# Kernel optimization log

Hardware: AMD Instinct MI355X
Metric: run time of the kernel (lower is better)

Reference implementation:

```python
import math
import jax, jax.numpy as jnp
import numpy as np

H = 8
D = 32  # c_hidden per head


def setup_inputs() -> dict:
    key = jax.random.key(0)
    ks = jax.random.split(key, 10)
    B, Q, K, C = 2, 2048, 2048, 256
    s = 1.0 / math.sqrt(C)
    return {
        "q_x": jax.random.normal(ks[0], (B, Q, C), jnp.float32),
        "kv_x": jax.random.normal(ks[1], (B, K, C), jnp.float32),
        "bias_mask": jax.random.normal(ks[2], (B, 1, 1, K), jnp.float32),
        "bias_pair": jax.random.normal(ks[3], (1, H, Q, K), jnp.float32),
        "Wq": jax.random.normal(ks[4], (H * D, C), jnp.float32) * s,
        "Wk": jax.random.normal(ks[5], (H * D, C), jnp.float32) * s,
        "Wv": jax.random.normal(ks[6], (H * D, C), jnp.float32) * s,
        "Wo": jax.random.normal(ks[7], (C, H * D), jnp.float32) * s,
        "bo": jnp.zeros((C,), jnp.float32),
        "Wg": jax.random.normal(ks[8], (H * D, C), jnp.float32) * s,
        "bg": jnp.zeros((H * D,), jnp.float32),
    }


def reference(q_x, kv_x, bias_mask, bias_pair, Wq, Wk, Wv, Wo, bo, Wg, bg):
    B, Q, C = q_x.shape
    K = kv_x.shape[-2]
    # projections (torch Linear: x @ W.T), split heads -> [B,H,L,D]
    q = (q_x @ Wq.T).reshape(B, Q, H, D).swapaxes(-2, -3) / math.sqrt(D)
    k = (kv_x @ Wk.T).reshape(B, K, H, D).swapaxes(-2, -3)
    v = (kv_x @ Wv.T).reshape(B, K, H, D).swapaxes(-2, -3)
    scores = jnp.einsum("bhqd,bhkd->bhqk", q, k) + bias_mask + bias_pair
    w = jax.nn.softmax(scores, axis=-1)
    o = jnp.einsum("bhqk,bhkd->bhqd", w, v).swapaxes(-2, -3)  # [B,Q,H,D]
    g = jax.nn.sigmoid(q_x @ Wg.T + bg).reshape(B, Q, H, D)
    o = o * g
    return o.reshape(B, Q, H * D) @ Wo.T + bo
```

## Files before the change

kernel.cpp:

```cpp
#include <hip/hip_runtime.h>
#include <hip/hip_bf16.h>
#include <stdint.h>
#include <math.h>

typedef __attribute__((ext_vector_type(8))) short bf16x8;
typedef __attribute__((ext_vector_type(4))) float f32x4;

#define HQ 2048
#define HK 2048
#define NH 8
#define ND 32
#define NC 256

union U8 { uint32_t u[4]; bf16x8 v; };

__device__ __forceinline__ uint16_t f2bf(float f) {
  uint32_t u = __float_as_uint(f);
  u += 0x7FFFu + ((u >> 16) & 1u);
  return (uint16_t)(u >> 16);
}
__device__ __forceinline__ uint32_t pack2bf(float a, float b) {
  return (uint32_t)f2bf(a) | ((uint32_t)f2bf(b) << 16);
}
__device__ __forceinline__ int swz64(int row, int piece) {
  int s = (((row >> 3) & 1) << 1) | ((row >> 1) & 1);
  return row * 64 + ((piece ^ s) << 4);
}
__device__ __forceinline__ f32x4 mfma32(bf16x8 a, bf16x8 b, f32x4 c) {
  return __builtin_amdgcn_mfma_f32_16x16x32_bf16(a, b, c, 0, 0, 0);
}
__device__ __forceinline__ void dma16(const void* g, void* l) {
  __builtin_amdgcn_global_load_lds(
      (const __attribute__((address_space(1))) uint32_t*)g,
      (__attribute__((address_space(3))) uint32_t*)l, 16, 0, 0);
}

__global__ __launch_bounds__(256) void proj_kernel(
    const float* __restrict__ qx, const float* __restrict__ kvx,
    const float* __restrict__ Wq, const float* __restrict__ Wk,
    const float* __restrict__ Wv, const float* __restrict__ Wg,
    const float* __restrict__ bg,
    uint16_t* __restrict__ q_p, uint16_t* __restrict__ k_p,
    uint16_t* __restrict__ v_p, float* __restrict__ g_ws)
{
  const int bx = blockIdx.x;
  const int Mb = bx & 63, Nb = (bx >> 6) & 3, p = bx >> 8;
  const int Mbase = Mb * 64, Nbase = Nb * 64;
  const float* X = (p == 0 || p == 3) ? qx : kvx;
  const float* W = (p == 0) ? Wq : (p == 1) ? Wk : (p == 2) ? Wv : Wg;

  __shared__ __align__(16) uint16_t smem[4096];
  uint16_t* sX = smem;
  uint16_t* sW = smem + 2048;

  const int tid = threadIdx.x;
  const int l = tid & 63, w = tid >> 6;
  const int qq = l & 15, g = l >> 4;
  const int row = tid >> 2, gp = tid & 3;

  f32x4 acc[4] = {};

  for (int ks = 0; ks < 8; ++ks) {
    const float* xs = X + (size_t)(Mbase + row) * 256 + ks * 32 + gp * 8;
    f32x4 x0 = *(const f32x4*)xs;
    f32x4 x1 = *(const f32x4*)(xs + 4);
    const float* ws_ = W + (size_t)(Nbase + row) * 256 + ks * 32 + gp * 8;
    f32x4 w0 = *(const f32x4*)ws_;
    f32x4 w1 = *(const f32x4*)(ws_ + 4);
    U8 ux, uw;
    ux.u[0] = pack2bf(x0[0], x0[1]); ux.u[1] = pack2bf(x0[2], x0[3]);
    ux.u[2] = pack2bf(x1[0], x1[1]); ux.u[3] = pack2bf(x1[2], x1[3]);
    uw.u[0] = pack2bf(w0[0], w0[1]); uw.u[1] = pack2bf(w0[2], w0[3]);
    uw.u[2] = pack2bf(w1[0], w1[1]); uw.u[3] = pack2bf(w1[2], w1[3]);
    __syncthreads();
    *(bf16x8*)((char*)sX + swz64(row, gp)) = ux.v;
    *(bf16x8*)((char*)sW + swz64(row, gp)) = uw.v;
    __syncthreads();
    bf16x8 a = *(bf16x8*)((char*)sX + swz64(w * 16 + qq, g));
#pragma unroll
    for (int nf = 0; nf < 4; ++nf) {
      bf16x8 bb = *(bf16x8*)((char*)sW + swz64(nf * 16 + qq, g));
      acc[nf] = mfma32(a, bb, acc[nf]);
    }
  }

  if (p == 2) {
    __syncthreads();
#pragma unroll
    for (int nf = 0; nf < 4; ++nf) {
      int n_loc = nf * 16 + qq;
#pragma unroll
      for (int r = 0; r < 4; ++r) {
        int m_loc = w * 16 + 4 * g + r;
        int byte = n_loc * 128 + ((((m_loc >> 3) ^ (n_loc & 7)) << 4)) + (m_loc & 7) * 2;
        *(uint16_t*)((char*)smem + byte) = f2bf(acc[nf][r]);
      }
    }
    __syncthreads();
    const int n_loc = tid >> 2, mp = tid & 3;
    const int ng = Nbase + n_loc;
    const int hh = ng >> 5, dd = ng & 31;
    const int bb_ = Mbase >> 11;
#pragma unroll
    for (int jj = 0; jj < 2; ++jj) {
      int piece = mp * 2 + jj;
      bf16x8 vv = *(bf16x8*)((char*)smem + n_loc * 128 + ((piece ^ (n_loc & 7)) << 4));
      int seq = (Mbase & 2047) + piece * 8;
      *(bf16x8*)(v_p + ((size_t)(bb_ * NH + hh) * ND + dd) * (size_t)HK + seq) = vv;
    }
    return;
  }

#pragma unroll
  for (int nf = 0; nf < 4; ++nf) {
    int n = Nbase + nf * 16 + qq;
#pragma unroll
    for (int r = 0; r < 4; ++r) {
      int m = Mbase + w * 16 + 4 * g + r;
      float val = acc[nf][r];
      if (p == 0) {
        val *= 0.17677669529663687f;
        int bb_ = m >> 11, seq = m & 2047, hh = n >> 5, dd = n & 31;
        q_p[((size_t)(bb_ * NH + hh) * HQ + seq) * ND + dd] = f2bf(val);
      } else if (p == 1) {
        int bb_ = m >> 11, seq = m & 2047, hh = n >> 5, dd = n & 31;
        k_p[((size_t)(bb_ * NH + hh) * HK + seq) * ND + dd] = f2bf(val);
      } else {
        g_ws[(size_t)m * NC + n] = 1.f / (1.f + __expf(-(val + bg[n])));
      }
    }
  }
}

__global__ __launch_bounds__(256, 2) void attn_kernel(
    const uint16_t* __restrict__ q_p, const uint16_t* __restrict__ k_p,
    const uint16_t* __restrict__ v_p, const float* __restrict__ bias_mask,
    const float* __restrict__ bias_pair,
    float* __restrict__ O_ws, float* __restrict__ l_ws)
{
  const int bx = blockIdx.x;
  const int kh = bx & 1, h = (bx >> 1) & 7, qt = bx >> 4;

  __shared__ __align__(16) char LDS[73728];
  char* sK = LDS;
  char* sV = LDS + 16384;
  char* sP = LDS + 32768;
  char* sBM = LDS + 65536;

  const int tid = threadIdx.x;
  const int l = tid & 63, wq = tid >> 6;
  const int qq = l & 15, g = l >> 4;
  const int q_glob = qt * 64 + wq * 16 + qq;

  bf16x8 qf0 = *(const bf16x8*)(q_p + ((size_t)h * HQ + q_glob) * ND + g * 8);
  bf16x8 qf1 = *(const bf16x8*)(q_p + ((size_t)(NH + h) * HQ + q_glob) * ND + g * 8);

  int kOffLane;
  {
    int B = wq * 1024 + l * 16;
    int Lr = B >> 7, q8 = l & 7;
    int hp = q8 ^ (Lr & 7);
    int half = hp >> 2, pc = hp & 3;
    int s = Lr * 2 + half, F = s >> 4, qs = s & 15;
    int krow = 8 * (qs >> 2) + (qs & 3) + (F & 1) * 4 + (F >> 1) * 32;
    kOffLane = krow * 64 + pc * 16;
  }
  const char* kSrc0 = (const char*)(k_p + (size_t)h * HK * ND) + kh * 65536 + kOffLane;
  const char* kSrc1 = (const char*)(k_p + (size_t)(NH + h) * HK * ND) + kh * 65536 + kOffLane;
  int vOffLane;
  {
    int B = wq * 1024 + l * 16;
    int d = B >> 7, q8 = l & 7;
    int pc = q8 ^ (d & 7);
    vOffLane = d * (HK * 2) + pc * 16;
  }
  const char* vSrc0 = (const char*)(v_p + (size_t)h * ND * (size_t)HK) + kh * 2048 + vOffLane;
  const char* vSrc1 = (const char*)(v_p + (size_t)(NH + h) * ND * (size_t)HK) + kh * 2048 + vOffLane;
  const char* pSrc0; const char* pSrc1; const char* pSrc2; const char* pSrc3;
  {
    const char* bpBlk = (const char*)bias_pair + ((size_t)h * HQ + qt * 64) * (size_t)HK * 4 + kh * 4096;
    int q16 = l & 15;
#define BP_SRC(jj) ({ int row = (wq * 4 + (jj)) * 4 + (l >> 4); \
                      int pc = (q16 & 8) | ((q16 & 7) ^ (row & 7)); \
                      bpBlk + (size_t)row * HK * 4 + pc * 16; })
    pSrc0 = BP_SRC(0); pSrc1 = BP_SRC(1); pSrc2 = BP_SRC(2); pSrc3 = BP_SRC(3);
#undef BP_SRC
  }

  int afOff[4], vaOff[4], bpOff[4];
#pragma unroll
  for (int F = 0; F < 4; ++F) {
    int Ls = 8 * F + (qq >> 1);
    afOff[F] = Ls * 128 + (((qq & 1) * 4 + g) ^ (qq >> 1)) * 16;
  }
#pragma unroll
  for (int hd = 0; hd < 2; ++hd)
#pragma unroll
    for (int c = 0; c < 2; ++c) {
      int d = hd * 16 + qq;
      vaOff[hd * 2 + c] = d * 128 + ((4 * c + g) ^ (d & 7)) * 16;
    }
#pragma unroll
  for (int F = 0; F < 4; ++F) {
    int piece = 8 * (F >> 1) + 2 * g + (F & 1);
    int row = wq * 16 + qq;
    bpOff[F] = row * 256 + ((piece & 8) | ((piece & 7) ^ (row & 7))) * 16;
  }

#define STAGE(tt, dbi) do { \
    dma16(kSrc0 + (size_t)(tt) * 4096, sK + (dbi) * 8192 + wq * 1024); \
    dma16(kSrc1 + (size_t)(tt) * 4096, sK + (dbi) * 8192 + 4096 + wq * 1024); \
    dma16(vSrc0 + (size_t)(tt) * 128,  sV + (dbi) * 8192 + wq * 1024); \
    dma16(vSrc1 + (size_t)(tt) * 128,  sV + (dbi) * 8192 + 4096 + wq * 1024); \
    dma16(pSrc0 + (size_t)(tt) * 256,  sP + (dbi) * 16384 + wq * 4096); \
    dma16(pSrc1 + (size_t)(tt) * 256,  sP + (dbi) * 16384 + wq * 4096 + 1024); \
    dma16(pSrc2 + (size_t)(tt) * 256,  sP + (dbi) * 16384 + wq * 4096 + 2048); \
    dma16(pSrc3 + (size_t)(tt) * 256,  sP + (dbi) * 16384 + wq * 4096 + 3072); \
  } while (0)

  f32x4 o00 = {}, o01 = {}, o10 = {}, o11 = {};
  float l0 = 0.f, l1 = 0.f;

  dma16((const char*)bias_mask + kh * 4096 + wq * 1024 + l * 16,
        sBM + wq * 1024);
  dma16((const char*)bias_mask + 8192 + kh * 4096 + wq * 1024 + l * 16,
        sBM + 4096 + wq * 1024);
  STAGE(0, 0);

#pragma unroll 1
  for (int t = 0; t < 16; ++t) {
    const int bi = t & 1;
    if (t < 15) {
      STAGE(t + 1, bi ^ 1);
      asm volatile("s_waitcnt vmcnt(8)" ::: "memory");
    } else {
      asm volatile("s_waitcnt vmcnt(0)" ::: "memory");
    }
    __builtin_amdgcn_s_barrier();
    __builtin_amdgcn_sched_barrier(0);

    const char* bP = sP + bi * 16384;
    f32x4 bp0 = *(const f32x4*)(bP + bpOff[0]);
    f32x4 bp1 = *(const f32x4*)(bP + bpOff[1]);
    f32x4 bp2 = *(const f32x4*)(bP + bpOff[2]);
    f32x4 bp3 = *(const f32x4*)(bP + bpOff[3]);
    const int bmOff = t * 256 + 32 * g;

    {
      const char* bK = sK + bi * 8192;
      const char* bV = sV + bi * 8192;
      bf16x8 af0 = *(const bf16x8*)(bK + afOff[0]);
      bf16x8 af1 = *(const bf16x8*)(bK + afOff[1]);
      bf16x8 af2 = *(const bf16x8*)(bK + afOff[2]);
      bf16x8 af3 = *(const bf16x8*)(bK + afOff[3]);
      f32x4 z = {};
      f32x4 s0 = mfma32(af0, qf0, z);
      f32x4 s1 = mfma32(af1, qf0, z);
      f32x4 s2 = mfma32(af2, qf0, z);
      f32x4 s3 = mfma32(af3, qf0, z);
      f32x4 bm0 = *(const f32x4*)(sBM + bmOff);
      f32x4 bm1 = *(const f32x4*)(sBM + bmOff + 16);
      f32x4 bm2 = *(const f32x4*)(sBM + bmOff + 128);
      f32x4 bm3 = *(const f32x4*)(sBM + bmOff + 144);
#pragma unroll
      for (int r = 0; r < 4; ++r) {
        s0[r] += bp0[r] + bm0[r];
        s1[r] += bp1[r] + bm1[r];
        s2[r] += bp2[r] + bm2[r];
        s3[r] += bp3[r] + bm3[r];
      }
      uint32_t pbk[4][2];
      {
        float p0 = __expf(s0[0]), p1 = __expf(s0[1]);
        float p2 = __expf(s0[2]), p3 = __expf(s0[3]);
        l0 += (p0 + p1) + (p2 + p3);
        pbk[0][0] = pack2bf(p0, p1); pbk[0][1] = pack2bf(p2, p3);
        p0 = __expf(s1[0]); p1 = __expf(s1[1]);
        p2 = __expf(s1[2]); p3 = __expf(s1[3]);
        l0 += (p0 + p1) + (p2 + p3);
        pbk[1][0] = pack2bf(p0, p1); pbk[1][1] = pack2bf(p2, p3);
        p0 = __expf(s2[0]); p1 = __expf(s2[1]);
        p2 = __expf(s2[2]); p3 = __expf(s2[3]);
        l0 += (p0 + p1) + (p2 + p3);
        pbk[2][0] = pack2bf(p0, p1); pbk[2][1] = pack2bf(p2, p3);
        p0 = __expf(s3[0]); p1 = __expf(s3[1]);
        p2 = __expf(s3[2]); p3 = __expf(s3[3]);
        l0 += (p0 + p1) + (p2 + p3);
        pbk[3][0] = pack2bf(p0, p1); pbk[3][1] = pack2bf(p2, p3);
      }
      U8 bu0, bu1;
      bu0.u[0] = pbk[0][0]; bu0.u[1] = pbk[0][1];
      bu0.u[2] = pbk[1][0]; bu0.u[3] = pbk[1][1];
      bu1.u[0] = pbk[2][0]; bu1.u[1] = pbk[2][1];
      bu1.u[2] = pbk[3][0]; bu1.u[3] = pbk[3][1];
      bf16x8 va00 = *(const bf16x8*)(bV + vaOff[0]);
      bf16x8 va01 = *(const bf16x8*)(bV + vaOff[1]);
      bf16x8 va10 = *(const bf16x8*)(bV + vaOff[2]);
      bf16x8 va11 = *(const bf16x8*)(bV + vaOff[3]);
      o00 = mfma32(va00, bu0.v, o00);
      o01 = mfma32(va10, bu0.v, o01);
      o00 = mfma32(va01, bu1.v, o00);
      o01 = mfma32(va11, bu1.v, o01);
    }
    {
      const char* bK = sK + bi * 8192 + 4096;
      const char* bV = sV + bi * 8192 + 4096;
      bf16x8 af0 = *(const bf16x8*)(bK + afOff[0]);
      bf16x8 af1 = *(const bf16x8*)(bK + afOff[1]);
      bf16x8 af2 = *(const bf16x8*)(bK + afOff[2]);
      bf16x8 af3 = *(const bf16x8*)(bK + afOff[3]);
      f32x4 z = {};
      f32x4 s0 = mfma32(af0, qf1, z);
      f32x4 s1 = mfma32(af1, qf1, z);
      f32x4 s2 = mfma32(af2, qf1, z);
      f32x4 s3 = mfma32(af3, qf1, z);
      f32x4 bm0 = *(const f32x4*)(sBM + 4096 + bmOff);
      f32x4 bm1 = *(const f32x4*)(sBM + 4096 + bmOff + 16);
      f32x4 bm2 = *(const f32x4*)(sBM + 4096 + bmOff + 128);
      f32x4 bm3 = *(const f32x4*)(sBM + 4096 + bmOff + 144);
#pragma unroll
      for (int r = 0; r < 4; ++r) {
        s0[r] += bp0[r] + bm0[r];
        s1[r] += bp1[r] + bm1[r];
        s2[r] += bp2[r] + bm2[r];
        s3[r] += bp3[r] + bm3[r];
      }
      uint32_t pbk[4][2];
      {
        float p0 = __expf(s0[0]), p1 = __expf(s0[1]);
        float p2 = __expf(s0[2]), p3 = __expf(s0[3]);
        l1 += (p0 + p1) + (p2 + p3);
        pbk[0][0] = pack2bf(p0, p1); pbk[0][1] = pack2bf(p2, p3);
        p0 = __expf(s1[0]); p1 = __expf(s1[1]);
        p2 = __expf(s1[2]); p3 = __expf(s1[3]);
        l1 += (p0 + p1) + (p2 + p3);
        pbk[1][0] = pack2bf(p0, p1); pbk[1][1] = pack2bf(p2, p3);
        p0 = __expf(s2[0]); p1 = __expf(s2[1]);
        p2 = __expf(s2[2]); p3 = __expf(s2[3]);
        l1 += (p0 + p1) + (p2 + p3);
        pbk[2][0] = pack2bf(p0, p1); pbk[2][1] = pack2bf(p2, p3);
        p0 = __expf(s3[0]); p1 = __expf(s3[1]);
        p2 = __expf(s3[2]); p3 = __expf(s3[3]);
        l1 += (p0 + p1) + (p2 + p3);
        pbk[3][0] = pack2bf(p0, p1); pbk[3][1] = pack2bf(p2, p3);
      }
      U8 bu0, bu1;
      bu0.u[0] = pbk[0][0]; bu0.u[1] = pbk[0][1];
      bu0.u[2] = pbk[1][0]; bu0.u[3] = pbk[1][1];
      bu1.u[0] = pbk[2][0]; bu1.u[1] = pbk[2][1];
      bu1.u[2] = pbk[3][0]; bu1.u[3] = pbk[3][1];
      bf16x8 va00 = *(const bf16x8*)(bV + vaOff[0]);
      bf16x8 va01 = *(const bf16x8*)(bV + vaOff[1]);
      bf16x8 va10 = *(const bf16x8*)(bV + vaOff[2]);
      bf16x8 va11 = *(const bf16x8*)(bV + vaOff[3]);
      o10 = mfma32(va00, bu0.v, o10);
      o11 = mfma32(va10, bu0.v, o11);
      o10 = mfma32(va01, bu1.v, o10);
      o11 = mfma32(va11, bu1.v, o11);
    }

    __builtin_amdgcn_sched_barrier(0);
    __builtin_amdgcn_s_barrier();
  }
#undef STAGE

  l0 += __shfl_xor(l0, 16, 64);
  l0 += __shfl_xor(l0, 32, 64);
  l1 += __shfl_xor(l1, 16, 64);
  l1 += __shfl_xor(l1, 32, 64);
#pragma unroll
  for (int b = 0; b < 2; ++b) {
    f32x4 oa = b ? o10 : o00;
    f32x4 ob = b ? o11 : o01;
    float lr = b ? l1 : l0;
    __syncthreads();
    float* se = (float*)LDS + wq * 576;
#pragma unroll
    for (int r = 0; r < 4; ++r) {
      se[qq * 36 + 4 * g + r]      = oa[r];
      se[qq * 36 + 16 + 4 * g + r] = ob[r];
    }
    if (g == 0) l_ws[kh * 32768 + b * 16384 + h * 2048 + q_glob] = lr;
    __syncthreads();
    const int qrow = l >> 2, pc = l & 3;
    const float* sr = (float*)LDS + wq * 576 + qrow * 36 + pc * 8;
    f32x4 x0 = *(const f32x4*)sr;
    f32x4 x1 = *(const f32x4*)(sr + 4);
    const int q_out = qt * 64 + wq * 16 + qrow;
    float* dst = O_ws + ((size_t)((kh * 2 + b) * HQ + q_out)) * NC + h * ND + pc * 8;
    *(f32x4*)dst = x0;
    *(f32x4*)(dst + 4) = x1;
  }
}

__global__ __launch_bounds__(256) void outproj_kernel(
    const float* __restrict__ O_ws, const float* __restrict__ l_ws,
    const float* __restrict__ g_ws, const float* __restrict__ Wo,
    const float* __restrict__ bo, float* __restrict__ out)
{
  const int bx = blockIdx.x;
  const int Mb = bx & 63, Nb = bx >> 6;
  const int Mbase = Mb * 64, Nbase = Nb * 64;
  __shared__ __align__(16) uint16_t smem2[4096];
  uint16_t* sA = smem2;
  uint16_t* sB = smem2 + 2048;
  const int tid = threadIdx.x;
  const int l = tid & 63, w = tid >> 6;
  const int qq = l & 15, g = l >> 4;
  const int row = tid >> 2, gp = tid & 3;
  const int m = Mbase + row, bb2 = m >> 11, qloc = m & 2047;
  f32x4 acc[4] = {};
  for (int ks = 0; ks < 8; ++ks) {
    const size_t lidx = (size_t)bb2 * 16384 + (size_t)ks * 2048 + qloc;
    const float inv = 1.f / (l_ws[lidx] + l_ws[32768 + lidx]);
    const int col = ks * 32 + gp * 8;
    const float* o0p = O_ws + ((size_t)(bb2 * HQ + qloc)) * NC + col;
    const float* o1p = O_ws + ((size_t)((2 + bb2) * HQ + qloc)) * NC + col;
    const float* gpp = g_ws + ((size_t)(bb2 * HQ + qloc)) * NC + col;
    f32x4 a0 = *(const f32x4*)o0p;      f32x4 a1 = *(const f32x4*)(o0p + 4);
    f32x4 b0 = *(const f32x4*)o1p;      f32x4 b1 = *(const f32x4*)(o1p + 4);
    f32x4 g0 = *(const f32x4*)gpp;      f32x4 g1 = *(const f32x4*)(gpp + 4);
#pragma unroll
    for (int r = 0; r < 4; ++r) {
      a0[r] = (a0[r] + b0[r]) * inv * g0[r];
      a1[r] = (a1[r] + b1[r]) * inv * g1[r];
    }
    const float* wsrc = Wo + (size_t)(Nbase + row) * 256 + ks * 32 + gp * 8;
    f32x4 w0 = *(const f32x4*)wsrc;
    f32x4 w1 = *(const f32x4*)(wsrc + 4);
    U8 ua, uw;
    ua.u[0] = pack2bf(a0[0], a0[1]); ua.u[1] = pack2bf(a0[2], a0[3]);
    ua.u[2] = pack2bf(a1[0], a1[1]); ua.u[3] = pack2bf(a1[2], a1[3]);
    uw.u[0] = pack2bf(w0[0], w0[1]); uw.u[1] = pack2bf(w0[2], w0[3]);
    uw.u[2] = pack2bf(w1[0], w1[1]); uw.u[3] = pack2bf(w1[2], w1[3]);
    __syncthreads();
    *(bf16x8*)((char*)sA + swz64(row, gp)) = ua.v;
    *(bf16x8*)((char*)sB + swz64(row, gp)) = uw.v;
    __syncthreads();
    bf16x8 a = *(bf16x8*)((char*)sA + swz64(w * 16 + qq, g));
#pragma unroll
    for (int nf = 0; nf < 4; ++nf) {
      bf16x8 bb = *(bf16x8*)((char*)sB + swz64(nf * 16 + qq, g));
      acc[nf] = mfma32(a, bb, acc[nf]);
    }
  }
#pragma unroll
  for (int nf = 0; nf < 4; ++nf) {
    int n = Nbase + nf * 16 + qq;
    float bias = bo[n];
#pragma unroll
    for (int r = 0; r < 4; ++r) {
      int mm = Mbase + w * 16 + 4 * g + r;
      out[(size_t)mm * NC + n] = acc[nf][r] + bias;
    }
  }
}

extern "C" void kernel_launch(void* const* d_in, const int* in_sizes, int n_in,
                              void* d_out, int out_size, void* d_ws, size_t ws_size,
                              hipStream_t stream) {
  (void)in_sizes; (void)n_in; (void)out_size; (void)ws_size;
  const float* qx        = (const float*)d_in[0];
  const float* kvx       = (const float*)d_in[1];
  const float* bias_mask = (const float*)d_in[2];
  const float* bias_pair = (const float*)d_in[3];
  const float* Wq        = (const float*)d_in[4];
  const float* Wk        = (const float*)d_in[5];
  const float* Wv        = (const float*)d_in[6];
  const float* Wo        = (const float*)d_in[7];
  const float* bo        = (const float*)d_in[8];
  const float* Wg        = (const float*)d_in[9];
  const float* bg        = (const float*)d_in[10];

  char* ws = (char*)d_ws;
  uint16_t* q_p  = (uint16_t*)(ws);
  uint16_t* k_p  = (uint16_t*)(ws + (2u << 20));
  uint16_t* v_p  = (uint16_t*)(ws + (4u << 20));
  float*    g_ws = (float*)   (ws + (6u << 20));
  float*    O_ws = (float*)   (ws + (10u << 20));
  float*    l_ws = (float*)   (ws + (18u << 20));
  float* out = (float*)d_out;

  proj_kernel<<<dim3(1024), dim3(256), 0, stream>>>(qx, kvx, Wq, Wk, Wv, Wg, bg,
                                                    q_p, k_p, v_p, g_ws);
  attn_kernel<<<dim3(512), dim3(256), 0, stream>>>(q_p, k_p, v_p, bias_mask,
                                                   bias_pair, O_ws, l_ws);
  outproj_kernel<<<dim3(256), dim3(256), 0, stream>>>(O_ws, l_ws, g_ws, Wo, bo, out);
}
```

Before: 57.46 us.

## Double attention block to 128 query rows with 8 waves sharing K/V tiles

The attention kernel now runs 512-thread blocks covering 128 queries instead of 256-thread blocks covering 64. The grid is halved, and each K/V tile staged into LDS is shared by eight waves instead of four. K and V staging is split across the wave halves, so each wave issues fewer DMA loads per iteration and the waitcnt threshold is lowered to match. The larger bias_pair buffer raises LDS use to about 104KB per block, which may cut occupancy to one block per CU and leaves only 256 blocks to spread across the GPU.

```diff
diff --git a/kernel.cpp b/kernel.cpp
--- a/kernel.cpp
+++ b/kernel.cpp
@@ -132,7 +132,7 @@
   }
 }
 
-__global__ __launch_bounds__(256, 2) void attn_kernel(
+__global__ __launch_bounds__(512, 2) void attn_kernel(
     const uint16_t* __restrict__ q_p, const uint16_t* __restrict__ k_p,
     const uint16_t* __restrict__ v_p, const float* __restrict__ bias_mask,
     const float* __restrict__ bias_pair,
@@ -141,48 +141,48 @@
   const int bx = blockIdx.x;
   const int kh = bx & 1, h = (bx >> 1) & 7, qt = bx >> 4;
 
-  __shared__ __align__(16) char LDS[73728];
+  __shared__ __align__(16) char LDS[106496];
   char* sK = LDS;
   char* sV = LDS + 16384;
   char* sP = LDS + 32768;
-  char* sBM = LDS + 65536;
+  char* sBM = LDS + 98304;
 
   const int tid = threadIdx.x;
   const int l = tid & 63, wq = tid >> 6;
   const int qq = l & 15, g = l >> 4;
-  const int q_glob = qt * 64 + wq * 16 + qq;
+  const int ws4 = wq & 3, bsel = wq >> 2;
+  const int q_glob = qt * 128 + wq * 16 + qq;
 
   bf16x8 qf0 = *(const bf16x8*)(q_p + ((size_t)h * HQ + q_glob) * ND + g * 8);
   bf16x8 qf1 = *(const bf16x8*)(q_p + ((size_t)(NH + h) * HQ + q_glob) * ND + g * 8);
 
-  int kOffLane;
+  const char* kSrc;
   {
-    int B = wq * 1024 + l * 16;
+    int B = ws4 * 1024 + l * 16;
     int Lr = B >> 7, q8 = l & 7;
     int hp = q8 ^ (Lr & 7);
     int half = hp >> 2, pc = hp & 3;
     int s = Lr * 2 + half, F = s >> 4, qs = s & 15;
     int krow = 8 * (qs >> 2) + (qs & 3) + (F & 1) * 4 + (F >> 1) * 32;
-    kOffLane = krow * 64 + pc * 16;
-  }
-  const char* kSrc0 = (const char*)(k_p + (size_t)h * HK * ND) + kh * 65536 + kOffLane;
-  const char* kSrc1 = (const char*)(k_p + (size_t)(NH + h) * HK * ND) + kh * 65536 + kOffLane;
-  int vOffLane;
+    kSrc = (const char*)(k_p + (size_t)(bsel * NH + h) * HK * ND)
+           + kh * 65536 + krow * 64 + pc * 16;
+  }
+  const char* vSrc;
   {
-    int B = wq * 1024 + l * 16;
+    int B = ws4 * 1024 + l * 16;
     int d = B >> 7, q8 = l & 7;
     int pc = q8 ^ (d & 7);
-    vOffLane = d * (HK * 2) + pc * 16;
-  }
-  const char* vSrc0 = (const char*)(v_p + (size_t)h * ND * (size_t)HK) + kh * 2048 + vOffLane;
-  const char* vSrc1 = (const char*)(v_p + (size_t)(NH + h) * ND * (size_t)HK) + kh * 2048 + vOffLane;
+    vSrc = (const char*)(v_p + (size_t)(bsel * NH + h) * ND * (size_t)HK)
+           + kh * 2048 + (size_t)d * (HK * 2) + pc * 16;
+  }
   const char* pSrc0; const char* pSrc1; const char* pSrc2; const char* pSrc3;
   {
-    const char* bpBlk = (const char*)bias_pair + ((size_t)h * HQ + qt * 64) * (size_t)HK * 4 + kh * 4096;
+    const char* bpBlk = (const char*)bias_pair
+        + ((size_t)h * HQ + qt * 128) * (size_t)HK * 4 + kh * 4096;
     int q16 = l & 15;
-#define BP_SRC(jj) ({ int row = (wq * 4 + (jj)) * 4 + (l >> 4); \
+#define BP_SRC(jj) ({ int row = wq * 16 + (jj) * 4 + (l >> 4); \
                       int pc = (q16 & 8) | ((q16 & 7) ^ (row & 7)); \
-                      bpBlk + (size_t)row * HK * 4 + pc * 16; })
+                      bpBlk + (size_t)row * (HK * 4) + pc * 16; })
     pSrc0 = BP_SRC(0); pSrc1 = BP_SRC(1); pSrc2 = BP_SRC(2); pSrc3 = BP_SRC(3);
 #undef BP_SRC
   }
@@ -208,23 +208,19 @@
   }
 
 #define STAGE(tt, dbi) do { \
-    dma16(kSrc0 + (size_t)(tt) * 4096, sK + (dbi) * 8192 + wq * 1024); \
-    dma16(kSrc1 + (size_t)(tt) * 4096, sK + (dbi) * 8192 + 4096 + wq * 1024); \
-    dma16(vSrc0 + (size_t)(tt) * 128,  sV + (dbi) * 8192 + wq * 1024); \
-    dma16(vSrc1 + (size_t)(tt) * 128,  sV + (dbi) * 8192 + 4096 + wq * 1024); \
-    dma16(pSrc0 + (size_t)(tt) * 256,  sP + (dbi) * 16384 + wq * 4096); \
-    dma16(pSrc1 + (size_t)(tt) * 256,  sP + (dbi) * 16384 + wq * 4096 + 1024); \
-    dma16(pSrc2 + (size_t)(tt) * 256,  sP + (dbi) * 16384 + wq * 4096 + 2048); \
-    dma16(pSrc3 + (size_t)(tt) * 256,  sP + (dbi) * 16384 + wq * 4096 + 3072); \
+    dma16(kSrc + (size_t)(tt) * 4096, sK + (dbi) * 8192 + bsel * 4096 + ws4 * 1024); \
+    dma16(vSrc + (size_t)(tt) * 128,  sV + (dbi) * 8192 + bsel * 4096 + ws4 * 1024); \
+    dma16(pSrc0 + (size_t)(tt) * 256, sP + (dbi) * 32768 + wq * 4096); \
+    dma16(pSrc1 + (size_t)(tt) * 256, sP + (dbi) * 32768 + wq * 4096 + 1024); \
+    dma16(pSrc2 + (size_t)(tt) * 256, sP + (dbi) * 32768 + wq * 4096 + 2048); \
+    dma16(pSrc3 + (size_t)(tt) * 256, sP + (dbi) * 32768 + wq * 4096 + 3072); \
   } while (0)
 
   f32x4 o00 = {}, o01 = {}, o10 = {}, o11 = {};
   float l0 = 0.f, l1 = 0.f;
 
-  dma16((const char*)bias_mask + kh * 4096 + wq * 1024 + l * 16,
-        sBM + wq * 1024);
-  dma16((const char*)bias_mask + 8192 + kh * 4096 + wq * 1024 + l * 16,
-        sBM + 4096 + wq * 1024);
+  dma16((const char*)bias_mask + bsel * 8192 + kh * 4096 + ws4 * 1024 + l * 16,
+        sBM + bsel * 4096 + ws4 * 1024);
   STAGE(0, 0);
 
 #pragma unroll 1
@@ -232,14 +228,14 @@
     const int bi = t & 1;
     if (t < 15) {
       STAGE(t + 1, bi ^ 1);
-      asm volatile("s_waitcnt vmcnt(8)" ::: "memory");
+      asm volatile("s_waitcnt vmcnt(6)" ::: "memory");
     } else {
       asm volatile("s_waitcnt vmcnt(0)" ::: "memory");
     }
     __builtin_amdgcn_s_barrier();
     __builtin_amdgcn_sched_barrier(0);
 
-    const char* bP = sP + bi * 16384;
+    const char* bP = sP + bi * 32768;
     f32x4 bp0 = *(const f32x4*)(bP + bpOff[0]);
     f32x4 bp1 = *(const f32x4*)(bP + bpOff[1]);
     f32x4 bp2 = *(const f32x4*)(bP + bpOff[2]);
@@ -386,7 +382,7 @@
     const float* sr = (float*)LDS + wq * 576 + qrow * 36 + pc * 8;
     f32x4 x0 = *(const f32x4*)sr;
     f32x4 x1 = *(const f32x4*)(sr + 4);
-    const int q_out = qt * 64 + wq * 16 + qrow;
+    const int q_out = qt * 128 + wq * 16 + qrow;
     float* dst = O_ws + ((size_t)((kh * 2 + b) * HQ + q_out)) * NC + h * ND + pc * 8;
     *(f32x4*)dst = x0;
     *(f32x4*)(dst + 4) = x1;
@@ -483,7 +479,7 @@
 
   proj_kernel<<<dim3(1024), dim3(256), 0, stream>>>(qx, kvx, Wq, Wk, Wv, Wg, bg,
                                                     q_p, k_p, v_p, g_ws);
-  attn_kernel<<<dim3(512), dim3(256), 0, stream>>>(q_p, k_p, v_p, bias_mask,
+  attn_kernel<<<dim3(256), dim3(512), 0, stream>>>(q_p, k_p, v_p, bias_mask,
                                                    bias_pair, O_ws, l_ws);
   outproj_kernel<<<dim3(256), dim3(256), 0, stream>>>(O_ws, l_ws, g_ws, Wo, bo, out);
 }
```

Measured after the change: 60.33 us. +5.0%, slower.
